# Kernel tuning notes

Hardware: AMD Instinct MI355X
Metric: run time of the kernel (lower is better)

Reference implementation:

```python
import jax, jax.numpy as jnp
import numpy as np

N_NODES = 40000


def _gcn_conv(x, edge_index, W, b):
    """PyG GCNConv: add self-loops, symmetric degree normalization,
    linear transform, gather-scale-scatter aggregation, bias."""
    n = x.shape[0]
    loops = jnp.arange(n, dtype=edge_index.dtype)
    src = jnp.concatenate([edge_index[0], loops])  # [E+N]
    dst = jnp.concatenate([edge_index[1], loops])  # [E+N]
    ones = jnp.ones(src.shape[0], dtype=x.dtype)
    deg = jax.ops.segment_sum(ones, dst, num_segments=n)  # in-degree incl. self-loop
    dinv = jnp.where(deg > 0, jax.lax.rsqrt(deg), 0.0)
    norm = dinv[src] * dinv[dst]  # [E+N]
    h = x @ W  # [n, out]
    msg = h[src] * norm[:, None]  # [E+N, out] gather + scale
    out = jax.ops.segment_sum(msg, dst, num_segments=n)  # scatter-add
    return out + b


def setup_inputs() -> dict:
    key = jax.random.key(0)
    k = jax.random.split(key, 6)
    n, din, dh, dout = N_NODES, 128, 128, 64
    x = jax.random.normal(k[0], (n, din), dtype=jnp.float32)
    edge_index = jax.random.randint(k[1], (2, 640000), 0, n, dtype=jnp.int64)
    W1 = jax.random.normal(k[2], (din, dh), dtype=jnp.float32) / np.sqrt(din)
    b1 = jnp.zeros((dh,), dtype=jnp.float32)
    W2 = jax.random.normal(k[3], (dh, dout), dtype=jnp.float32) / np.sqrt(dh)
    b2 = jnp.zeros((dout,), dtype=jnp.float32)
    return {"x": x, "edge_index": edge_index, "W1": W1, "b1": b1, "W2": W2, "b2": b2}


def reference(x, edge_index, W1, b1, W2, b2):
    h = jax.nn.relu(_gcn_conv(x, edge_index, W1, b1))
    return _gcn_conv(h, edge_index, W2, b2)
```

## Files before the change

### kernel.cpp

```cpp
#include <hip/hip_runtime.h>
#include <hip/hip_fp16.h>


#define N_NODES 40000
#define DIN 128
#define DH 128
#define DOUT 64
#define NEDGES 640000
#define CAP 64
#define NBUCKET 2560
#define I4_PER_CHUNK 500
#define NODES_PER_XCD 5000

typedef _Float16 f16x8 __attribute__((ext_vector_type(8)));
typedef float f32x4 __attribute__((ext_vector_type(4)));

__global__ void k_init(int* __restrict__ deg, const float* __restrict__ W1,
                       const float* __restrict__ W2,
                       _Float16* __restrict__ WT1, _Float16* __restrict__ WT2, int n) {
    int i = blockIdx.x * 256 + threadIdx.x;
    if (i < n) deg[i] = 0;
    if (i < DIN * DH) {
        int k = i >> 7, nn = i & 127;
        WT1[(size_t)nn * DIN + k] = (_Float16)W1[i];
    }
    if (i < DH * DOUT) {
        int k = i >> 6, nn = i & 63;
        WT2[(size_t)nn * DH + k] = (_Float16)W2[i];
    }
}

__global__ __launch_bounds__(256) void k_work1(
    const float* __restrict__ x, const _Float16* __restrict__ WT,
    __half* __restrict__ h,
    const int4* __restrict__ src4, const int4* __restrict__ dst4,
    int* __restrict__ deg, unsigned short* __restrict__ ssrc)
{
    if (blockIdx.x < NBUCKET) {
        const int xg = blockIdx.x & 7;
        const int c  = blockIdx.x >> 3;
        const int lo = xg * NODES_PER_XCD, hi = lo + NODES_PER_XCD;
        const int e0 = c * I4_PER_CHUNK, e1 = e0 + I4_PER_CHUNK;
        for (int e = e0 + threadIdx.x; e < e1; e += 256) {
            int4 d = dst4[e];
            int4 s = src4[e];
            if (d.x >= lo && d.x < hi) {
                int p = atomicAdd(&deg[d.x], 1);
                if (p < CAP) ssrc[d.x * CAP + p] = (unsigned short)s.x;
            }
            if (d.y >= lo && d.y < hi) {
                int p = atomicAdd(&deg[d.y], 1);
                if (p < CAP) ssrc[d.y * CAP + p] = (unsigned short)s.y;
            }
            if (d.z >= lo && d.z < hi) {
                int p = atomicAdd(&deg[d.z], 1);
                if (p < CAP) ssrc[d.z * CAP + p] = (unsigned short)s.z;
            }
            if (d.w >= lo && d.w < hi) {
                int p = atomicAdd(&deg[d.w], 1);
                if (p < CAP) ssrc[d.w * CAP + p] = (unsigned short)s.w;
            }
        }
    } else {
        const int wave = (blockIdx.x - NBUCKET) * 4 + (threadIdx.x >> 6);
        const int lane = threadIdx.x & 63;
        const int m = lane & 15, quad = lane >> 4;

        f32x4 acc[8];
#pragma unroll
        for (int nt = 0; nt < 8; ++nt) acc[nt] = (f32x4){0.f, 0.f, 0.f, 0.f};

        const float* xrow = x + (size_t)(wave * 16 + m) * DIN + quad * 8;
#pragma unroll
        for (int ks = 0; ks < 4; ++ks) {
            float4 xa = *(const float4*)(xrow + ks * 32);
            float4 xb = *(const float4*)(xrow + ks * 32 + 4);
            f16x8 a = { (_Float16)xa.x, (_Float16)xa.y, (_Float16)xa.z, (_Float16)xa.w,
                        (_Float16)xb.x, (_Float16)xb.y, (_Float16)xb.z, (_Float16)xb.w };
#pragma unroll
            for (int nt = 0; nt < 8; ++nt) {
                f16x8 b = *(const f16x8*)(WT + (size_t)(nt * 16 + m) * DIN + ks * 32 + quad * 8);
                acc[nt] = __builtin_amdgcn_mfma_f32_16x16x32_f16(a, b, acc[nt], 0, 0, 0);
            }
        }
#pragma unroll
        for (int r = 0; r < 4; ++r) {
            int orow = wave * 16 + quad * 4 + r;
#pragma unroll
            for (int nt = 0; nt < 8; ++nt)
                h[(size_t)orow * DH + nt * 16 + m] = (__half)acc[nt][r];
        }
    }
}

__global__ __launch_bounds__(1024) void k_agg1g2(
    const int* __restrict__ deg, const unsigned short* __restrict__ ssrc,
    const __half* __restrict__ h1, const float* __restrict__ b1,
    const _Float16* __restrict__ WT2, __half* __restrict__ h2)
{
    __shared__ _Float16 xs[16][136];
    const int w = threadIdx.x >> 6;
    const int lane = threadIdx.x & 63;
    const int node0 = blockIdx.x * 16;
    const int node = node0 + w;
    const __half2* hp = (const __half2*)h1;

    const int dg = deg[node];
    const int cnt = min(dg, CAP);
    const float dn = rsqrtf((float)(dg + 1));
    float2 self = __half22float2(hp[(size_t)node * 64 + lane]);
    float2 acc = { self.x * dn, self.y * dn };
    int sv = (lane < cnt) ? (int)ssrc[node * CAP + lane] : 0;
    float dval = (lane < cnt) ? rsqrtf((float)(deg[sv] + 1)) : 0.f;
    int e = 0;
    for (; e + 8 <= cnt; e += 8) {
        int s0 = __shfl(sv, e),     s1 = __shfl(sv, e + 1);
        int s2 = __shfl(sv, e + 2), s3 = __shfl(sv, e + 3);
        int s4 = __shfl(sv, e + 4), s5 = __shfl(sv, e + 5);
        int s6 = __shfl(sv, e + 6), s7 = __shfl(sv, e + 7);
        float w0 = __shfl(dval, e),     w1 = __shfl(dval, e + 1);
        float w2 = __shfl(dval, e + 2), w3 = __shfl(dval, e + 3);
        float w4 = __shfl(dval, e + 4), w5 = __shfl(dval, e + 5);
        float w6 = __shfl(dval, e + 6), w7 = __shfl(dval, e + 7);
        float2 v0 = __half22float2(hp[(size_t)s0 * 64 + lane]);
        float2 v1 = __half22float2(hp[(size_t)s1 * 64 + lane]);
        float2 v2 = __half22float2(hp[(size_t)s2 * 64 + lane]);
        float2 v3 = __half22float2(hp[(size_t)s3 * 64 + lane]);
        float2 v4 = __half22float2(hp[(size_t)s4 * 64 + lane]);
        float2 v5 = __half22float2(hp[(size_t)s5 * 64 + lane]);
        float2 v6 = __half22float2(hp[(size_t)s6 * 64 + lane]);
        float2 v7 = __half22float2(hp[(size_t)s7 * 64 + lane]);
        acc.x += (v0.x * w0 + v1.x * w1) + (v2.x * w2 + v3.x * w3)
               + (v4.x * w4 + v5.x * w5) + (v6.x * w6 + v7.x * w7);
        acc.y += (v0.y * w0 + v1.y * w1) + (v2.y * w2 + v3.y * w3)
               + (v4.y * w4 + v5.y * w5) + (v6.y * w6 + v7.y * w7);
    }
    for (; e < cnt; ++e) {
        int s = __shfl(sv, e);
        float wv = __shfl(dval, e);
        float2 v = __half22float2(hp[(size_t)s * 64 + lane]);
        acc.x += v.x * wv; acc.y += v.y * wv;
    }
    float vx = dn * acc.x + b1[2 * lane];
    float vy = dn * acc.y + b1[2 * lane + 1];
    xs[w][2 * lane]     = (_Float16)(vx > 0.f ? vx : 0.f);
    xs[w][2 * lane + 1] = (_Float16)(vy > 0.f ? vy : 0.f);
    __syncthreads();

    if (w < 4) {
        const int m = lane & 15, quad = lane >> 4;
        f32x4 acc2 = (f32x4){0.f, 0.f, 0.f, 0.f};
#pragma unroll
        for (int ks = 0; ks < 4; ++ks) {
            f16x8 a = *(const f16x8*)&xs[m][ks * 32 + quad * 8];
            f16x8 b = *(const f16x8*)(WT2 + (size_t)(w * 16 + m) * DH + ks * 32 + quad * 8);
            acc2 = __builtin_amdgcn_mfma_f32_16x16x32_f16(a, b, acc2, 0, 0, 0);
        }
#pragma unroll
        for (int r = 0; r < 4; ++r) {
            int nrow = node0 + quad * 4 + r;
            float dnr = rsqrtf((float)(deg[nrow] + 1));
            h2[(size_t)nrow * DOUT + w * 16 + m] = (__half)(acc2[r] * dnr);
        }
    }
}

__global__ __launch_bounds__(256) void k_agg2(
    const int* __restrict__ deg, const unsigned short* __restrict__ ssrc,
    const __half* __restrict__ h, const float* __restrict__ b2,
    float* __restrict__ out)
{
    const int node = blockIdx.x * 4 + (threadIdx.x >> 6);
    const int lane = threadIdx.x & 63;
    const int half = lane >> 5;
    const int lp = lane & 31;
    const int dg = deg[node];
    const int cnt = min(dg, CAP);
    const __half2* hp = (const __half2*)h;

    float2 acc;
    if (half == 0) acc = __half22float2(hp[(size_t)node * 32 + lp]);
    else           acc = make_float2(0.f, 0.f);

    int sv = (lane < cnt) ? (int)ssrc[node * CAP + lane] : 0;
    int e = 0;
    for (; e + 16 <= cnt; e += 16) {
        int b = e + half;
        int s0 = __shfl(sv, b),      s1 = __shfl(sv, b + 2);
        int s2 = __shfl(sv, b + 4),  s3 = __shfl(sv, b + 6);
        int s4 = __shfl(sv, b + 8),  s5 = __shfl(sv, b + 10);
        int s6 = __shfl(sv, b + 12), s7 = __shfl(sv, b + 14);
        float2 v0 = __half22float2(hp[(size_t)s0 * 32 + lp]);
        float2 v1 = __half22float2(hp[(size_t)s1 * 32 + lp]);
        float2 v2 = __half22float2(hp[(size_t)s2 * 32 + lp]);
        float2 v3 = __half22float2(hp[(size_t)s3 * 32 + lp]);
        float2 v4 = __half22float2(hp[(size_t)s4 * 32 + lp]);
        float2 v5 = __half22float2(hp[(size_t)s5 * 32 + lp]);
        float2 v6 = __half22float2(hp[(size_t)s6 * 32 + lp]);
        float2 v7 = __half22float2(hp[(size_t)s7 * 32 + lp]);
        acc.x += ((v0.x + v1.x) + (v2.x + v3.x)) + ((v4.x + v5.x) + (v6.x + v7.x));
        acc.y += ((v0.y + v1.y) + (v2.y + v3.y)) + ((v4.y + v5.y) + (v6.y + v7.y));
    }
    for (; e + 2 <= cnt; e += 2) {
        int s = __shfl(sv, e + half);
        float2 v = __half22float2(hp[(size_t)s * 32 + lp]);
        acc.x += v.x; acc.y += v.y;
    }
    if (e < cnt) {
        int s = __shfl(sv, e);
        if (half == 0) {
            float2 v = __half22float2(hp[(size_t)s * 32 + lp]);
            acc.x += v.x; acc.y += v.y;
        }
    }
    acc.x += __shfl_xor(acc.x, 32);
    acc.y += __shfl_xor(acc.y, 32);
    if (half == 0) {
        float dn = rsqrtf((float)(dg + 1));
        float2 o;
        o.x = dn * acc.x + b2[2 * lp];
        o.y = dn * acc.y + b2[2 * lp + 1];
        *(float2*)&out[(size_t)node * 64 + 2 * lp] = o;
    }
}

extern "C" void kernel_launch(void* const* d_in, const int* in_sizes, int n_in,
                              void* d_out, int out_size, void* d_ws, size_t ws_size,
                              hipStream_t stream) {
    const float* x  = (const float*)d_in[0];
    const int*   ei = (const int*)d_in[1];
    const float* W1 = (const float*)d_in[2];
    const float* b1 = (const float*)d_in[3];
    const float* W2 = (const float*)d_in[4];
    const float* b2 = (const float*)d_in[5];
    float* out = (float*)d_out;

    const int n = N_NODES, E = NEDGES;
    const int* src = ei;
    const int* dst = ei + E;

    char* ws = (char*)d_ws;
    int*            deg  = (int*)(ws + 0);
    _Float16*       WT1  = (_Float16*)(ws + 163840);
    _Float16*       WT2  = (_Float16*)(ws + 196608);
    unsigned short* ssrc = (unsigned short*)(ws + 212992);
    __half*         h1   = (__half*)(ws + 5332992);
    __half*         h2   = (__half*)(ws + 15572992);

    k_init   <<<(n + 255) / 256, 256, 0, stream>>>(deg, W1, W2, WT1, WT2, n);
    k_work1  <<<NBUCKET + 625, 256, 0, stream>>>(x, WT1, h1, (const int4*)src,
                                                 (const int4*)dst, deg, ssrc);
    k_agg1g2 <<<n / 16, 1024, 0, stream>>>(deg, ssrc, h1, b1, WT2, h2);
    k_agg2   <<<n / 4,  256, 0, stream>>>(deg, ssrc, h2, b2, out);
}
```

Measured before the change: 179.3 us.

## Aggregate raw features before first GEMM and fuse layer-1 GEMM into aggregation

New measurement: 171.9 us. 1.04x faster.

```diff
diff --git a/kernel.cpp b/kernel.cpp
--- a/kernel.cpp
+++ b/kernel.cpp
@@ -11,6 +11,7 @@
 #define NBUCKET 2560
 #define I4_PER_CHUNK 500
 #define NODES_PER_XCD 5000
+#define NCVT 1250
 
 typedef _Float16 f16x8 __attribute__((ext_vector_type(8)));
 typedef float f32x4 __attribute__((ext_vector_type(4)));
@@ -30,9 +31,8 @@
     }
 }
 
-__global__ __launch_bounds__(256) void k_work1(
-    const float* __restrict__ x, const _Float16* __restrict__ WT,
-    __half* __restrict__ h,
+__global__ __launch_bounds__(256) void k_bkt_cvt(
+    const float* __restrict__ x, _Float16* __restrict__ xh,
     const int4* __restrict__ src4, const int4* __restrict__ dst4,
     int* __restrict__ deg, unsigned short* __restrict__ ssrc)
 {
@@ -62,48 +62,33 @@
             }
         }
     } else {
-        const int wave = (blockIdx.x - NBUCKET) * 4 + (threadIdx.x >> 6);
-        const int lane = threadIdx.x & 63;
-        const int m = lane & 15, quad = lane >> 4;
-
-        f32x4 acc[8];
-#pragma unroll
-        for (int nt = 0; nt < 8; ++nt) acc[nt] = (f32x4){0.f, 0.f, 0.f, 0.f};
-
-        const float* xrow = x + (size_t)(wave * 16 + m) * DIN + quad * 8;
-#pragma unroll
-        for (int ks = 0; ks < 4; ++ks) {
-            float4 xa = *(const float4*)(xrow + ks * 32);
-            float4 xb = *(const float4*)(xrow + ks * 32 + 4);
-            f16x8 a = { (_Float16)xa.x, (_Float16)xa.y, (_Float16)xa.z, (_Float16)xa.w,
-                        (_Float16)xb.x, (_Float16)xb.y, (_Float16)xb.z, (_Float16)xb.w };
-#pragma unroll
-            for (int nt = 0; nt < 8; ++nt) {
-                f16x8 b = *(const f16x8*)(WT + (size_t)(nt * 16 + m) * DIN + ks * 32 + quad * 8);
-                acc[nt] = __builtin_amdgcn_mfma_f32_16x16x32_f16(a, b, acc[nt], 0, 0, 0);
-            }
-        }
-#pragma unroll
-        for (int r = 0; r < 4; ++r) {
-            int orow = wave * 16 + quad * 4 + r;
-#pragma unroll
-            for (int nt = 0; nt < 8; ++nt)
-                h[(size_t)orow * DH + nt * 16 + m] = (__half)acc[nt][r];
-        }
-    }
-}
-
-__global__ __launch_bounds__(1024) void k_agg1g2(
+        const size_t base = ((size_t)(blockIdx.x - NBUCKET) * 256 + threadIdx.x) * 16;
+        float4 a0 = *(const float4*)(x + base);
+        float4 a1 = *(const float4*)(x + base + 4);
+        float4 a2 = *(const float4*)(x + base + 8);
+        float4 a3 = *(const float4*)(x + base + 12);
+        f16x8 o0 = { (_Float16)a0.x, (_Float16)a0.y, (_Float16)a0.z, (_Float16)a0.w,
+                     (_Float16)a1.x, (_Float16)a1.y, (_Float16)a1.z, (_Float16)a1.w };
+        f16x8 o1 = { (_Float16)a2.x, (_Float16)a2.y, (_Float16)a2.z, (_Float16)a2.w,
+                     (_Float16)a3.x, (_Float16)a3.y, (_Float16)a3.z, (_Float16)a3.w };
+        *(f16x8*)(xh + base)     = o0;
+        *(f16x8*)(xh + base + 8) = o1;
+    }
+}
+
+__global__ __launch_bounds__(1024) void k_agg_g12(
     const int* __restrict__ deg, const unsigned short* __restrict__ ssrc,
-    const __half* __restrict__ h1, const float* __restrict__ b1,
-    const _Float16* __restrict__ WT2, __half* __restrict__ h2)
+    const __half* __restrict__ xh, const float* __restrict__ b1,
+    const _Float16* __restrict__ WT1, const _Float16* __restrict__ WT2,
+    __half* __restrict__ h2)
 {
-    __shared__ _Float16 xs[16][136];
+    __shared__ _Float16 ys[16][136];
+    __shared__ _Float16 zs[16][136];
     const int w = threadIdx.x >> 6;
     const int lane = threadIdx.x & 63;
     const int node0 = blockIdx.x * 16;
     const int node = node0 + w;
-    const __half2* hp = (const __half2*)h1;
+    const __half2* hp = (const __half2*)xh;
 
     const int dg = deg[node];
     const int cnt = min(dg, CAP);
@@ -141,18 +126,33 @@
         float2 v = __half22float2(hp[(size_t)s * 64 + lane]);
         acc.x += v.x * wv; acc.y += v.y * wv;
     }
-    float vx = dn * acc.x + b1[2 * lane];
-    float vy = dn * acc.y + b1[2 * lane + 1];
-    xs[w][2 * lane]     = (_Float16)(vx > 0.f ? vx : 0.f);
-    xs[w][2 * lane + 1] = (_Float16)(vy > 0.f ? vy : 0.f);
+    ys[w][2 * lane]     = (_Float16)(dn * acc.x);
+    ys[w][2 * lane + 1] = (_Float16)(dn * acc.y);
     __syncthreads();
 
+    const int m = lane & 15, quad = lane >> 4;
+    if (w < 8) {
+        f32x4 acc1 = (f32x4){0.f, 0.f, 0.f, 0.f};
+#pragma unroll
+        for (int ks = 0; ks < 4; ++ks) {
+            f16x8 a = *(const f16x8*)&ys[m][ks * 32 + quad * 8];
+            f16x8 b = *(const f16x8*)(WT1 + (size_t)(w * 16 + m) * DIN + ks * 32 + quad * 8);
+            acc1 = __builtin_amdgcn_mfma_f32_16x16x32_f16(a, b, acc1, 0, 0, 0);
+        }
+        float bias = b1[w * 16 + m];
+#pragma unroll
+        for (int r = 0; r < 4; ++r) {
+            float v = acc1[r] + bias;
+            zs[quad * 4 + r][w * 16 + m] = (_Float16)(v > 0.f ? v : 0.f);
+        }
+    }
+    __syncthreads();
+
     if (w < 4) {
-        const int m = lane & 15, quad = lane >> 4;
         f32x4 acc2 = (f32x4){0.f, 0.f, 0.f, 0.f};
 #pragma unroll
         for (int ks = 0; ks < 4; ++ks) {
-            f16x8 a = *(const f16x8*)&xs[m][ks * 32 + quad * 8];
+            f16x8 a = *(const f16x8*)&zs[m][ks * 32 + quad * 8];
             f16x8 b = *(const f16x8*)(WT2 + (size_t)(w * 16 + m) * DH + ks * 32 + quad * 8);
             acc2 = __builtin_amdgcn_mfma_f32_16x16x32_f16(a, b, acc2, 0, 0, 0);
         }
@@ -244,12 +244,13 @@
     _Float16*       WT1  = (_Float16*)(ws + 163840);
     _Float16*       WT2  = (_Float16*)(ws + 196608);
     unsigned short* ssrc = (unsigned short*)(ws + 212992);
-    __half*         h1   = (__half*)(ws + 5332992);
+    _Float16*       xh   = (_Float16*)(ws + 5332992);
     __half*         h2   = (__half*)(ws + 15572992);
 
-    k_init   <<<(n + 255) / 256, 256, 0, stream>>>(deg, W1, W2, WT1, WT2, n);
-    k_work1  <<<NBUCKET + 625, 256, 0, stream>>>(x, WT1, h1, (const int4*)src,
-                                                 (const int4*)dst, deg, ssrc);
-    k_agg1g2 <<<n / 16, 1024, 0, stream>>>(deg, ssrc, h1, b1, WT2, h2);
-    k_agg2   <<<n / 4,  256, 0, stream>>>(deg, ssrc, h2, b2, out);
-}
+    k_init    <<<(n + 255) / 256, 256, 0, stream>>>(deg, W1, W2, WT1, WT2, n);
+    k_bkt_cvt <<<NBUCKET + NCVT, 256, 0, stream>>>(x, xh, (const int4*)src,
+                                                   (const int4*)dst, deg, ssrc);
+    k_agg_g12 <<<n / 16, 1024, 0, stream>>>(deg, ssrc, (const __half*)xh, b1,
+                                            WT1, WT2, h2);
+    k_agg2    <<<n / 4,  256, 0, stream>>>(deg, ssrc, h2, b2, out);
+}
```

## Prescale h1 by source degree norm and read packed neighbor indices directly

Applied to the files above, without the earlier changes.

After: 180.1 us. About the same (+0.4%).

```diff
diff --git a/kernel.cpp b/kernel.cpp
--- a/kernel.cpp
+++ b/kernel.cpp
@@ -8,8 +8,8 @@
 #define DOUT 64
 #define NEDGES 640000
 #define CAP 64
-#define NBUCKET 2560
-#define I4_PER_CHUNK 500
+#define NBUCKET 640
+#define I4_PER_CHUNK 2000
 #define NODES_PER_XCD 5000
 
 typedef _Float16 f16x8 __attribute__((ext_vector_type(8)));
@@ -93,6 +93,19 @@
     }
 }
 
+__global__ __launch_bounds__(256) void k_scale(
+    __half* __restrict__ h1, const int* __restrict__ deg)
+{
+    int idx = blockIdx.x * 256 + threadIdx.x;
+    int row = idx >> 4;
+    float dn = rsqrtf((float)(deg[row] + 1));
+    f16x8 v = *(f16x8*)((_Float16*)h1 + (size_t)idx * 8);
+    f16x8 o;
+#pragma unroll
+    for (int j = 0; j < 8; ++j) o[j] = (_Float16)((float)v[j] * dn);
+    *(f16x8*)((_Float16*)h1 + (size_t)idx * 8) = o;
+}
+
 __global__ __launch_bounds__(1024) void k_agg1g2(
     const int* __restrict__ deg, const unsigned short* __restrict__ ssrc,
     const __half* __restrict__ h1, const float* __restrict__ b1,
@@ -108,20 +121,15 @@
     const int dg = deg[node];
     const int cnt = min(dg, CAP);
     const float dn = rsqrtf((float)(dg + 1));
-    float2 self = __half22float2(hp[(size_t)node * 64 + lane]);
-    float2 acc = { self.x * dn, self.y * dn };
-    int sv = (lane < cnt) ? (int)ssrc[node * CAP + lane] : 0;
-    float dval = (lane < cnt) ? rsqrtf((float)(deg[sv] + 1)) : 0.f;
+    float2 acc = __half22float2(hp[(size_t)node * 64 + lane]);
+    const uint4* bin4 = (const uint4*)(ssrc + node * CAP);
     int e = 0;
     for (; e + 8 <= cnt; e += 8) {
-        int s0 = __shfl(sv, e),     s1 = __shfl(sv, e + 1);
-        int s2 = __shfl(sv, e + 2), s3 = __shfl(sv, e + 3);
-        int s4 = __shfl(sv, e + 4), s5 = __shfl(sv, e + 5);
-        int s6 = __shfl(sv, e + 6), s7 = __shfl(sv, e + 7);
-        float w0 = __shfl(dval, e),     w1 = __shfl(dval, e + 1);
-        float w2 = __shfl(dval, e + 2), w3 = __shfl(dval, e + 3);
-        float w4 = __shfl(dval, e + 4), w5 = __shfl(dval, e + 5);
-        float w6 = __shfl(dval, e + 6), w7 = __shfl(dval, e + 7);
+        uint4 pk = bin4[e >> 3];
+        int s0 = pk.x & 0xFFFF, s1 = pk.x >> 16;
+        int s2 = pk.y & 0xFFFF, s3 = pk.y >> 16;
+        int s4 = pk.z & 0xFFFF, s5 = pk.z >> 16;
+        int s6 = pk.w & 0xFFFF, s7 = pk.w >> 16;
         float2 v0 = __half22float2(hp[(size_t)s0 * 64 + lane]);
         float2 v1 = __half22float2(hp[(size_t)s1 * 64 + lane]);
         float2 v2 = __half22float2(hp[(size_t)s2 * 64 + lane]);
@@ -130,16 +138,13 @@
         float2 v5 = __half22float2(hp[(size_t)s5 * 64 + lane]);
         float2 v6 = __half22float2(hp[(size_t)s6 * 64 + lane]);
         float2 v7 = __half22float2(hp[(size_t)s7 * 64 + lane]);
-        acc.x += (v0.x * w0 + v1.x * w1) + (v2.x * w2 + v3.x * w3)
-               + (v4.x * w4 + v5.x * w5) + (v6.x * w6 + v7.x * w7);
-        acc.y += (v0.y * w0 + v1.y * w1) + (v2.y * w2 + v3.y * w3)
-               + (v4.y * w4 + v5.y * w5) + (v6.y * w6 + v7.y * w7);
+        acc.x += ((v0.x + v1.x) + (v2.x + v3.x)) + ((v4.x + v5.x) + (v6.x + v7.x));
+        acc.y += ((v0.y + v1.y) + (v2.y + v3.y)) + ((v4.y + v5.y) + (v6.y + v7.y));
     }
     for (; e < cnt; ++e) {
-        int s = __shfl(sv, e);
-        float wv = __shfl(dval, e);
+        int s = ssrc[node * CAP + e];
         float2 v = __half22float2(hp[(size_t)s * 64 + lane]);
-        acc.x += v.x * wv; acc.y += v.y * wv;
+        acc.x += v.x; acc.y += v.y;
     }
     float vx = dn * acc.x + b1[2 * lane];
     float vy = dn * acc.y + b1[2 * lane + 1];
@@ -182,32 +187,29 @@
     if (half == 0) acc = __half22float2(hp[(size_t)node * 32 + lp]);
     else           acc = make_float2(0.f, 0.f);
 
-    int sv = (lane < cnt) ? (int)ssrc[node * CAP + lane] : 0;
+    const uint4* bin4 = (const uint4*)(ssrc + node * CAP);
     int e = 0;
-    for (; e + 16 <= cnt; e += 16) {
-        int b = e + half;
-        int s0 = __shfl(sv, b),      s1 = __shfl(sv, b + 2);
-        int s2 = __shfl(sv, b + 4),  s3 = __shfl(sv, b + 6);
-        int s4 = __shfl(sv, b + 8),  s5 = __shfl(sv, b + 10);
-        int s6 = __shfl(sv, b + 12), s7 = __shfl(sv, b + 14);
-        float2 v0 = __half22float2(hp[(size_t)s0 * 32 + lp]);
-        float2 v1 = __half22float2(hp[(size_t)s1 * 32 + lp]);
-        float2 v2 = __half22float2(hp[(size_t)s2 * 32 + lp]);
-        float2 v3 = __half22float2(hp[(size_t)s3 * 32 + lp]);
-        float2 v4 = __half22float2(hp[(size_t)s4 * 32 + lp]);
-        float2 v5 = __half22float2(hp[(size_t)s5 * 32 + lp]);
-        float2 v6 = __half22float2(hp[(size_t)s6 * 32 + lp]);
-        float2 v7 = __half22float2(hp[(size_t)s7 * 32 + lp]);
-        acc.x += ((v0.x + v1.x) + (v2.x + v3.x)) + ((v4.x + v5.x) + (v6.x + v7.x));
-        acc.y += ((v0.y + v1.y) + (v2.y + v3.y)) + ((v4.y + v5.y) + (v6.y + v7.y));
+    for (; e + 8 <= cnt; e += 8) {
+        uint4 pk = bin4[e >> 3];
+        int sa, sb, sc, sd;
+        if (half == 0) { sa = pk.x & 0xFFFF; sb = pk.y & 0xFFFF;
+                         sc = pk.z & 0xFFFF; sd = pk.w & 0xFFFF; }
+        else           { sa = pk.x >> 16;    sb = pk.y >> 16;
+                         sc = pk.z >> 16;    sd = pk.w >> 16; }
+        float2 v0 = __half22float2(hp[(size_t)sa * 32 + lp]);
+        float2 v1 = __half22float2(hp[(size_t)sb * 32 + lp]);
+        float2 v2 = __half22float2(hp[(size_t)sc * 32 + lp]);
+        float2 v3 = __half22float2(hp[(size_t)sd * 32 + lp]);
+        acc.x += (v0.x + v1.x) + (v2.x + v3.x);
+        acc.y += (v0.y + v1.y) + (v2.y + v3.y);
     }
     for (; e + 2 <= cnt; e += 2) {
-        int s = __shfl(sv, e + half);
+        int s = ssrc[node * CAP + e + half];
         float2 v = __half22float2(hp[(size_t)s * 32 + lp]);
         acc.x += v.x; acc.y += v.y;
     }
     if (e < cnt) {
-        int s = __shfl(sv, e);
+        int s = ssrc[node * CAP + e];
         if (half == 0) {
             float2 v = __half22float2(hp[(size_t)s * 32 + lp]);
             acc.x += v.x; acc.y += v.y;
@@ -250,6 +252,7 @@
     k_init   <<<(n + 255) / 256, 256, 0, stream>>>(deg, W1, W2, WT1, WT2, n);
     k_work1  <<<NBUCKET + 625, 256, 0, stream>>>(x, WT1, h1, (const int4*)src,
                                                  (const int4*)dst, deg, ssrc);
+    k_scale  <<<(N_NODES * DH / 8) / 256, 256, 0, stream>>>(h1, deg);
     k_agg1g2 <<<n / 16, 1024, 0, stream>>>(deg, ssrc, h1, b1, WT2, h2);
     k_agg2   <<<n / 4,  256, 0, stream>>>(deg, ssrc, h2, b2, out);
 }
```
